# Performance work log

Hardware: AMD Instinct MI355X
Metric: run time of the kernel (lower is better)

Reference implementation:

```python
import jax, jax.numpy as jnp
import numpy as np

N = 8192
D = 512
EPS = 1e-12  # F.normalize default eps


def setup_inputs() -> dict:
    key = jax.random.key(0)
    k1, k2 = jax.random.split(key)
    cur = jax.random.normal(k1, (N, D), dtype=jnp.float32)
    # randn -> mixed-sign entries, so every row of (incidence_m > 0) is unique
    # (the only case where the original `incidence_m += head` shapes agree).
    incidence_m = jax.random.normal(k2, (N, N), dtype=jnp.float32)
    return {"cur": cur, "incidence_m": incidence_m}


def reference(cur, incidence_m):
    # construct_directed: dedup rows of (incidence_m > 0); with all rows unique,
    # each node is its own hyperedge leader and head == mask as float, row order
    # preserved. head is built from python ints in torch, hence non-differentiable.
    mask = incidence_m > 0
    head = jax.lax.stop_gradient(mask.astype(incidence_m.dtype))  # [N, N]
    # F.normalize(head, dim=-1): L2 per row with eps clamp
    head = head / jnp.maximum(
        jnp.sqrt(jnp.sum(head * head, axis=-1, keepdims=True)), EPS
    )
    inc = incidence_m + head                          # [N, N]
    edge_fea = inc @ cur                              # [N, D]
    edge_degree = jnp.sum(inc, axis=-1, keepdims=True)  # [N, 1]
    return edge_fea / edge_degree
```

## Files before the change

### kernel.cpp

```cpp
#include <hip/hip_runtime.h>
#include <stdint.h>


#define NROWS 8192
#define DDIM  512

typedef float f32x4 __attribute__((ext_vector_type(4)));
typedef short s16x8 __attribute__((ext_vector_type(8)));

__device__ __forceinline__ unsigned short f2bf(float f) {
  union { float f; unsigned int u; } c; c.f = f;
  unsigned int u = c.u;
  unsigned int r = u + 0x7FFFu + ((u >> 16) & 1u);
  return (unsigned short)(r >> 16);
}

__global__ __launch_bounds__(256) void bprep_kernel(const float* __restrict__ cur,
                                                    unsigned char* __restrict__ bws) {
  int idx = blockIdx.x * 256 + threadIdx.x;
  int n = idx & 511;
  int kg9 = idx >> 9;
  int kt = kg9 >> 3;
  int kg = kg9 & 7;
  int k0 = kt * 64 + kg * 8;
  union { unsigned short h[8]; uint4 q; } u;
#pragma unroll
  for (int e = 0; e < 8; ++e)
    u.h[e] = f2bf(cur[(size_t)(k0 + e) * DDIM + n]);
  int nt = n >> 8, nn = n & 255;
  size_t off = ((size_t)(nt * 128 + kt) << 15) + ((size_t)kg << 12) + ((size_t)nn << 4);
  *(uint4*)(bws + off) = u.q;
}


#define FENCE() __builtin_amdgcn_sched_barrier(0)
#define BARRIER() __builtin_amdgcn_s_barrier()
#define WAITLGKM() asm volatile("s_waitcnt lgkmcnt(0)" ::: "memory")
#define MFMA_ __builtin_amdgcn_mfma_f32_16x16x32_bf16

__global__ __launch_bounds__(512, 4) void gemm_kernel(const float* __restrict__ inc,
                                                      const unsigned char* __restrict__ bws,
                                                      float* __restrict__ out) {
  __shared__ __align__(16) unsigned char smem[32768];
  unsigned char* const buf0 = smem;
  unsigned char* const buf1 = smem + 8192;
  unsigned char* const buf2 = smem + 16384;
  unsigned char* const buf3 = smem + 24576;

  const int tid = threadIdx.x;
  const int lane = tid & 63;
  const int wv = tid >> 6;
  const int r = lane & 15;
  const int q = lane >> 4;

  const int id = blockIdx.x;
  const int nt = (id & 7) >> 2;
  const int mt = (id >> 3) * 4 + (id & 3);
  const int brow = mt * 32;

  const int sm = tid >> 4;
  const int sp = tid & 15;
  const int kgw = sp >> 1, half = sp & 1;
  const float4* gAr = (const float4*)(inc + (size_t)(brow + sm) * NROWS) + sp;
  const int aWr = (kgw << 9) + ((sm ^ kgw) << 4) + (half << 3);

  int aOff[2][2];
#pragma unroll
  for (int kh = 0; kh < 2; ++kh)
#pragma unroll
    for (int rg = 0; rg < 2; ++rg) {
      int kg = kh * 4 + q;
      int row = rg * 16 + r;
      aOff[kh][rg] = (kg << 9) + ((row ^ kg) << 4);
    }

  const unsigned char* gB = bws + ((size_t)(nt * 128) << 15);
  int bOff[4];
#pragma unroll
  for (int kh = 0; kh < 2; ++kh)
#pragma unroll
    for (int cg = 0; cg < 2; ++cg)
      bOff[kh * 2 + cg] = ((kh * 4 + q) << 12) + ((wv * 32 + cg * 16 + r) << 4);

  f32x4 acc1[2][2], acc2[2][2];
#pragma unroll
  for (int a = 0; a < 2; ++a)
#pragma unroll
    for (int b = 0; b < 2; ++b) {
      acc1[a][b] = (f32x4){0.f, 0.f, 0.f, 0.f};
      acc2[a][b] = (f32x4){0.f, 0.f, 0.f, 0.f};
    }

  double s1 = 0.0;
  int cnt = 0;
  float4 x, y;
  s16x8 bX[4], bY[4];

#define ISSUE_A(d, KT) do { d = gAr[(KT) * 16]; } while (0)

#define LOADB(BS, KT) do {                                                                \
    const unsigned char* _g = gB + ((size_t)(KT) << 15);                                  \
    BS[0] = *(const s16x8*)(_g + bOff[0]);                                                \
    BS[1] = *(const s16x8*)(_g + bOff[1]);                                                \
    BS[2] = *(const s16x8*)(_g + bOff[2]);                                                \
    BS[3] = *(const s16x8*)(_g + bOff[3]);                                                \
  } while (0)

#define XFORM(v, BUF) do {                                                                \
    s1 += (double)v.x + (double)v.y + (double)v.z + (double)v.w;                          \
    cnt += (v.x > 0.f) + (v.y > 0.f) + (v.z > 0.f) + (v.w > 0.f);                         \
    unsigned dlo, dhi;                                                                    \
    asm("v_cvt_pk_bf16_f32 %0, %1, %2" : "=v"(dlo) : "v"(v.x), "v"(v.y));                 \
    asm("v_cvt_pk_bf16_f32 %0, %1, %2" : "=v"(dhi) : "v"(v.z), "v"(v.w));                 \
    unsigned mlo = (v.x > 0.f ? 0x3F80u : 0u) | (v.y > 0.f ? 0x3F800000u : 0u);           \
    unsigned mhi = (v.z > 0.f ? 0x3F80u : 0u) | (v.w > 0.f ? 0x3F800000u : 0u);           \
    *(unsigned long long*)((BUF) + aWr) =                                                 \
        (unsigned long long)dlo | ((unsigned long long)dhi << 32);                        \
    *(unsigned long long*)((BUF) + 4096 + aWr) =                                          \
        (unsigned long long)mlo | ((unsigned long long)mhi << 32);                        \
  } while (0)

#define MFMA_TILE(BUF, BS) do {                                                           \
    _Pragma("unroll")                                                                     \
    for (int kh = 0; kh < 2; ++kh) {                                                      \
      s16x8 af0 = *(const s16x8*)((BUF) + aOff[kh][0]);                                   \
      s16x8 af1 = *(const s16x8*)((BUF) + aOff[kh][1]);                                   \
      s16x8 mf0 = *(const s16x8*)((BUF) + 4096 + aOff[kh][0]);                            \
      s16x8 mf1 = *(const s16x8*)((BUF) + 4096 + aOff[kh][1]);                            \
      __builtin_amdgcn_s_setprio(1);                                                      \
      acc1[0][0] = MFMA_(af0, BS[kh * 2 + 0], acc1[0][0], 0, 0, 0);                       \
      acc2[0][0] = MFMA_(mf0, BS[kh * 2 + 0], acc2[0][0], 0, 0, 0);                       \
      acc1[0][1] = MFMA_(af0, BS[kh * 2 + 1], acc1[0][1], 0, 0, 0);                       \
      acc2[0][1] = MFMA_(mf0, BS[kh * 2 + 1], acc2[0][1], 0, 0, 0);                       \
      acc1[1][0] = MFMA_(af1, BS[kh * 2 + 0], acc1[1][0], 0, 0, 0);                       \
      acc2[1][0] = MFMA_(mf1, BS[kh * 2 + 0], acc2[1][0], 0, 0, 0);                       \
      acc1[1][1] = MFMA_(af1, BS[kh * 2 + 1], acc1[1][1], 0, 0, 0);                       \
      acc2[1][1] = MFMA_(mf1, BS[kh * 2 + 1], acc2[1][1], 0, 0, 0);                       \
      __builtin_amdgcn_s_setprio(0);                                                      \
    }                                                                                     \
  } while (0)

#define SYNC() do { FENCE(); WAITLGKM(); FENCE(); BARRIER(); FENCE(); } while (0)

  ISSUE_A(x, 0);
  ISSUE_A(y, 1);
  LOADB(bX, 0);
  XFORM(x, buf0);
  XFORM(y, buf1);
  SYNC();

  for (int i = 0; i < 31; ++i) {
    const int t = i * 4;
    ISSUE_A(x, t + 2);
    ISSUE_A(y, t + 3);
    LOADB(bY, t + 1);
    FENCE();
    MFMA_TILE(buf0, bX);
    XFORM(x, buf2);
    LOADB(bX, t + 2);
    FENCE();
    MFMA_TILE(buf1, bY);
    XFORM(y, buf3);
    SYNC();
    ISSUE_A(x, t + 4);
    ISSUE_A(y, t + 5);
    LOADB(bY, t + 3);
    FENCE();
    MFMA_TILE(buf2, bX);
    XFORM(x, buf0);
    LOADB(bX, t + 4);
    FENCE();
    MFMA_TILE(buf3, bY);
    XFORM(y, buf1);
    SYNC();
  }

  ISSUE_A(x, 126);
  ISSUE_A(y, 127);
  LOADB(bY, 125);
  FENCE();
  MFMA_TILE(buf0, bX);
  XFORM(x, buf2);
  LOADB(bX, 126);
  FENCE();
  MFMA_TILE(buf1, bY);
  XFORM(y, buf3);
  SYNC();
  LOADB(bY, 127);
  FENCE();
  MFMA_TILE(buf2, bX);
  FENCE();
  MFMA_TILE(buf3, bY);

#pragma unroll
  for (int o = 1; o < 16; o <<= 1) {
    s1 += __shfl_xor(s1, o);
    cnt += __shfl_xor(cnt, o);
  }
  __syncthreads();
  float* const invsS = (float*)buf0;
  float* const rdegS = invsS + 32;
  if (sp == 0) {
    double sq = sqrt((double)cnt);
    invsS[sm] = (cnt > 0) ? (float)(1.0 / sq) : 0.0f;
    rdegS[sm] = (float)(1.0 / (s1 + sq));
  }
  __syncthreads();

#pragma unroll
  for (int rg = 0; rg < 2; ++rg) {
#pragma unroll
    for (int cg = 0; cg < 2; ++cg) {
#pragma unroll
      for (int j = 0; j < 4; ++j) {
        int row = rg * 16 + q * 4 + j;
        out[(size_t)(brow + row) * DDIM + nt * 256 + wv * 32 + cg * 16 + r] =
            (acc1[rg][cg][j] + invsS[row] * acc2[rg][cg][j]) * rdegS[row];
      }
    }
  }
#undef ISSUE_A
#undef LOADB
#undef XFORM
#undef MFMA_TILE
#undef SYNC
}

extern "C" void kernel_launch(void* const* d_in, const int* in_sizes, int n_in,
                              void* d_out, int out_size, void* d_ws, size_t ws_size,
                              hipStream_t stream) {
  const float* cur = (const float*)d_in[0];
  const float* incm = (const float*)d_in[1];
  float* out = (float*)d_out;
  unsigned char* bws = (unsigned char*)d_ws;

  hipLaunchKernelGGL(bprep_kernel, dim3((NROWS * DDIM / 8) / 256), dim3(256), 0, stream,
                     cur, bws);
  hipLaunchKernelGGL(gemm_kernel, dim3(512), dim3(512), 0, stream, incm, bws, out);
}
```

Measured before the change: 172.5 us.

## Precompute row stats in separate pass and fold normalized mask into A operand

Adds a stats kernel that reads the incidence matrix once to compute per-row sums and positive counts, producing the inverse norm and reciprocal degree. The GEMM then adds the scaled mask to each element before bf16 conversion, so it needs only one accumulator set, half the MFMAs and half the LDS A tile. The cost is an extra full pass over the large incidence matrix and a kernel launch. Folding before rounding also changes bf16 rounding slightly.

```diff
diff --git a/kernel.cpp b/kernel.cpp
--- a/kernel.cpp
+++ b/kernel.cpp
@@ -13,6 +13,38 @@
   unsigned int u = c.u;
   unsigned int r = u + 0x7FFFu + ((u >> 16) & 1u);
   return (unsigned short)(r >> 16);
+}
+
+__global__ __launch_bounds__(256) void stats_kernel(const float* __restrict__ inc,
+                                                    float* __restrict__ invs,
+                                                    float* __restrict__ rdeg) {
+  int row = blockIdx.x;
+  int tid = threadIdx.x;
+  const float4* p = (const float4*)(inc + (size_t)row * NROWS);
+  double s = 0.0;
+  int c = 0;
+#pragma unroll
+  for (int i = 0; i < 8; ++i) {
+    float4 v = p[i * 256 + tid];
+    s += (double)v.x + (double)v.y + (double)v.z + (double)v.w;
+    c += (v.x > 0.f) + (v.y > 0.f) + (v.z > 0.f) + (v.w > 0.f);
+  }
+  for (int off = 32; off > 0; off >>= 1) {
+    s += __shfl_down(s, off);
+    c += __shfl_down(c, off);
+  }
+  __shared__ double sw[4];
+  __shared__ int cw[4];
+  int lane = tid & 63, wv = tid >> 6;
+  if (lane == 0) { sw[wv] = s; cw[wv] = c; }
+  __syncthreads();
+  if (tid == 0) {
+    double S = sw[0] + sw[1] + sw[2] + sw[3];
+    int C = cw[0] + cw[1] + cw[2] + cw[3];
+    double sq = sqrt((double)C);
+    invs[row] = (C > 0) ? (float)(1.0 / sq) : 0.0f;
+    rdeg[row] = (float)(1.0 / (S + sq));
+  }
 }
 
 __global__ __launch_bounds__(256) void bprep_kernel(const float* __restrict__ cur,
@@ -40,12 +72,15 @@
 
 __global__ __launch_bounds__(512, 4) void gemm_kernel(const float* __restrict__ inc,
                                                       const unsigned char* __restrict__ bws,
+                                                      const float* __restrict__ invs,
+                                                      const float* __restrict__ rdeg,
                                                       float* __restrict__ out) {
-  __shared__ __align__(16) unsigned char smem[32768];
+  __shared__ __align__(16) unsigned char smem[16512];
   unsigned char* const buf0 = smem;
-  unsigned char* const buf1 = smem + 8192;
-  unsigned char* const buf2 = smem + 16384;
-  unsigned char* const buf3 = smem + 24576;
+  unsigned char* const buf1 = smem + 4096;
+  unsigned char* const buf2 = smem + 8192;
+  unsigned char* const buf3 = smem + 12288;
+  float* const rdegS = (float*)(smem + 16384);
 
   const int tid = threadIdx.x;
   const int lane = tid & 63;
@@ -58,10 +93,13 @@
   const int mt = (id >> 3) * 4 + (id & 3);
   const int brow = mt * 32;
 
+  if (tid < 32) rdegS[tid] = rdeg[brow + tid];
+
   const int sm = tid >> 4;
   const int sp = tid & 15;
   const int kgw = sp >> 1, half = sp & 1;
   const float4* gAr = (const float4*)(inc + (size_t)(brow + sm) * NROWS) + sp;
+  const float invr = invs[brow + sm];
   const int aWr = (kgw << 9) + ((sm ^ kgw) << 4) + (half << 3);
 
   int aOff[2][2];
@@ -82,17 +120,13 @@
     for (int cg = 0; cg < 2; ++cg)
       bOff[kh * 2 + cg] = ((kh * 4 + q) << 12) + ((wv * 32 + cg * 16 + r) << 4);
 
-  f32x4 acc1[2][2], acc2[2][2];
+  f32x4 acc[2][2];
 #pragma unroll
   for (int a = 0; a < 2; ++a)
 #pragma unroll
-    for (int b = 0; b < 2; ++b) {
-      acc1[a][b] = (f32x4){0.f, 0.f, 0.f, 0.f};
-      acc2[a][b] = (f32x4){0.f, 0.f, 0.f, 0.f};
-    }
-
-  double s1 = 0.0;
-  int cnt = 0;
+    for (int b = 0; b < 2; ++b)
+      acc[a][b] = (f32x4){0.f, 0.f, 0.f, 0.f};
+
   float4 x, y;
   s16x8 bX[4], bY[4];
 
@@ -107,17 +141,15 @@
   } while (0)
 
 #define XFORM(v, BUF) do {                                                                \
-    s1 += (double)v.x + (double)v.y + (double)v.z + (double)v.w;                          \
-    cnt += (v.x > 0.f) + (v.y > 0.f) + (v.z > 0.f) + (v.w > 0.f);                         \
+    float a0 = v.x + (v.x > 0.f ? invr : 0.f);                                            \
+    float a1 = v.y + (v.y > 0.f ? invr : 0.f);                                            \
+    float a2 = v.z + (v.z > 0.f ? invr : 0.f);                                            \
+    float a3 = v.w + (v.w > 0.f ? invr : 0.f);                                            \
     unsigned dlo, dhi;                                                                    \
-    asm("v_cvt_pk_bf16_f32 %0, %1, %2" : "=v"(dlo) : "v"(v.x), "v"(v.y));                 \
-    asm("v_cvt_pk_bf16_f32 %0, %1, %2" : "=v"(dhi) : "v"(v.z), "v"(v.w));                 \
-    unsigned mlo = (v.x > 0.f ? 0x3F80u : 0u) | (v.y > 0.f ? 0x3F800000u : 0u);           \
-    unsigned mhi = (v.z > 0.f ? 0x3F80u : 0u) | (v.w > 0.f ? 0x3F800000u : 0u);           \
+    asm("v_cvt_pk_bf16_f32 %0, %1, %2" : "=v"(dlo) : "v"(a0), "v"(a1));                   \
+    asm("v_cvt_pk_bf16_f32 %0, %1, %2" : "=v"(dhi) : "v"(a2), "v"(a3));                   \
     *(unsigned long long*)((BUF) + aWr) =                                                 \
         (unsigned long long)dlo | ((unsigned long long)dhi << 32);                        \
-    *(unsigned long long*)((BUF) + 4096 + aWr) =                                          \
-        (unsigned long long)mlo | ((unsigned long long)mhi << 32);                        \
   } while (0)
 
 #define MFMA_TILE(BUF, BS) do {                                                           \
@@ -125,17 +157,11 @@
     for (int kh = 0; kh < 2; ++kh) {                                                      \
       s16x8 af0 = *(const s16x8*)((BUF) + aOff[kh][0]);                                   \
       s16x8 af1 = *(const s16x8*)((BUF) + aOff[kh][1]);                                   \
-      s16x8 mf0 = *(const s16x8*)((BUF) + 4096 + aOff[kh][0]);                            \
-      s16x8 mf1 = *(const s16x8*)((BUF) + 4096 + aOff[kh][1]);                            \
       __builtin_amdgcn_s_setprio(1);                                                      \
-      acc1[0][0] = MFMA_(af0, BS[kh * 2 + 0], acc1[0][0], 0, 0, 0);                       \
-      acc2[0][0] = MFMA_(mf0, BS[kh * 2 + 0], acc2[0][0], 0, 0, 0);                       \
-      acc1[0][1] = MFMA_(af0, BS[kh * 2 + 1], acc1[0][1], 0, 0, 0);                       \
-      acc2[0][1] = MFMA_(mf0, BS[kh * 2 + 1], acc2[0][1], 0, 0, 0);                       \
-      acc1[1][0] = MFMA_(af1, BS[kh * 2 + 0], acc1[1][0], 0, 0, 0);                       \
-      acc2[1][0] = MFMA_(mf1, BS[kh * 2 + 0], acc2[1][0], 0, 0, 0);                       \
-      acc1[1][1] = MFMA_(af1, BS[kh * 2 + 1], acc1[1][1], 0, 0, 0);                       \
-      acc2[1][1] = MFMA_(mf1, BS[kh * 2 + 1], acc2[1][1], 0, 0, 0);                       \
+      acc[0][0] = MFMA_(af0, BS[kh * 2 + 0], acc[0][0], 0, 0, 0);                         \
+      acc[0][1] = MFMA_(af0, BS[kh * 2 + 1], acc[0][1], 0, 0, 0);                         \
+      acc[1][0] = MFMA_(af1, BS[kh * 2 + 0], acc[1][0], 0, 0, 0);                         \
+      acc[1][1] = MFMA_(af1, BS[kh * 2 + 1], acc[1][1], 0, 0, 0);                         \
       __builtin_amdgcn_s_setprio(0);                                                      \
     }                                                                                     \
   } while (0)
@@ -193,21 +219,6 @@
   MFMA_TILE(buf3, bY);
 
 #pragma unroll
-  for (int o = 1; o < 16; o <<= 1) {
-    s1 += __shfl_xor(s1, o);
-    cnt += __shfl_xor(cnt, o);
-  }
-  __syncthreads();
-  float* const invsS = (float*)buf0;
-  float* const rdegS = invsS + 32;
-  if (sp == 0) {
-    double sq = sqrt((double)cnt);
-    invsS[sm] = (cnt > 0) ? (float)(1.0 / sq) : 0.0f;
-    rdegS[sm] = (float)(1.0 / (s1 + sq));
-  }
-  __syncthreads();
-
-#pragma unroll
   for (int rg = 0; rg < 2; ++rg) {
 #pragma unroll
     for (int cg = 0; cg < 2; ++cg) {
@@ -215,7 +226,7 @@
       for (int j = 0; j < 4; ++j) {
         int row = rg * 16 + q * 4 + j;
         out[(size_t)(brow + row) * DDIM + nt * 256 + wv * 32 + cg * 16 + r] =
-            (acc1[rg][cg][j] + invsS[row] * acc2[rg][cg][j]) * rdegS[row];
+            acc[rg][cg][j] * rdegS[row];
       }
     }
   }
@@ -232,9 +243,13 @@
   const float* cur = (const float*)d_in[0];
   const float* incm = (const float*)d_in[1];
   float* out = (float*)d_out;
-  unsigned char* bws = (unsigned char*)d_ws;
-
+  unsigned char* ws = (unsigned char*)d_ws;
+  float* invs = (float*)ws;
+  float* rdeg = (float*)(ws + 32768);
+  unsigned char* bws = ws + 65536;
+
+  hipLaunchKernelGGL(stats_kernel, dim3(NROWS), dim3(256), 0, stream, incm, invs, rdeg);
   hipLaunchKernelGGL(bprep_kernel, dim3((NROWS * DDIM / 8) / 256), dim3(256), 0, stream,
                      cur, bws);
-  hipLaunchKernelGGL(gemm_kernel, dim3(512), dim3(512), 0, stream, incm, bws, out);
-}
+  hipLaunchKernelGGL(gemm_kernel, dim3(512), dim3(512), 0, stream, incm, bws, invs, rdeg, out);
+}
```

Result: slower. 177.2 us (+2.7%).
